# Kernel optimization log

Hardware: AMD Instinct MI355X
Metric: run time of the kernel (lower is better)

## Reference

```python
import jax, jax.numpy as jnp
import numpy as np

B, N, D, DH = 8, 2048, 1024, 64

def setup_inputs() -> dict:
    key = jax.random.key(0)
    ks = jax.random.split(key, 4)
    s = 1.0 / np.sqrt(D)
    return {
        "x": jax.random.normal(ks[0], (B, N, D), dtype=jnp.float32),
        "Wq": jax.random.normal(ks[1], (D, DH), dtype=jnp.float32) * s,
        "bq": jnp.zeros((DH,), dtype=jnp.float32),
        "Wk": jax.random.normal(ks[2], (D, DH), dtype=jnp.float32) * s,
        "bk": jnp.zeros((DH,), dtype=jnp.float32),
        "Wv": jax.random.normal(ks[3], (D, DH), dtype=jnp.float32) * s,
        "bv": jnp.zeros((DH,), dtype=jnp.float32),
    }

def reference(x, Wq, bq, Wk, bk, Wv, bv):
    # Projections: [B,N,DH]
    Q = x @ Wq + bq
    K = x @ Wk + bk
    V = x @ Wv + bv
    sqrt_dh = jnp.sqrt(jnp.asarray(DH, dtype=x.dtype))
    # scores[b,i,j] = Q_i . K_j  (original materializes [B,N,N,DH]; GEMM is equivalent math)
    att = jnp.einsum("bid,bjd->bij", Q, K) / sqrt_dh
    # NOTE: original softmaxes over dim=1 (the query/i axis), not the usual j axis.
    att = jax.nn.softmax(att, axis=1)
    # Dropout is identity in eval mode.
    return jnp.einsum("bij,bjd->bid", att, V)
```

## Files before the change

### kernel.cpp

```cpp
#include <hip/hip_runtime.h>
#include <math.h>

#define Bn  8
#define Nn  2048
#define Dn  1024
#define DHn 64

typedef __attribute__((ext_vector_type(8))) short bf16x8;
typedef __attribute__((ext_vector_type(4))) float f32x4;

static __device__ inline short f2bf(float f) {
    unsigned u = __builtin_bit_cast(unsigned, f);
    u += 0x7FFFu + ((u >> 16) & 1u);
    return (short)(u >> 16);
}
static __device__ inline bf16x8 pack8(float4 a, float4 b) {
    bf16x8 v;
    v[0] = f2bf(a.x); v[1] = f2bf(a.y); v[2] = f2bf(a.z); v[3] = f2bf(a.w);
    v[4] = f2bf(b.x); v[5] = f2bf(b.y); v[6] = f2bf(b.z); v[7] = f2bf(b.w);
    return v;
}

__global__ __launch_bounds__(256) void wt_kernel(
    const float* __restrict__ Wq, const float* __restrict__ Wk,
    const float* __restrict__ Wv, short* __restrict__ Wt)
{
    const int gn = blockIdx.x;
    const float* Wm = (gn < 64) ? Wq : (gn < 128 ? Wk : Wv);
    const int n = gn & 63;
    const int t = threadIdx.x;
#pragma unroll
    for (int r = 0; r < 4; ++r) {
        const int k = t * 4 + r;
        Wt[gn * Dn + k] = f2bf(Wm[k * DHn + n]);
    }
}

__global__ __launch_bounds__(256) void zero_kernel(float* __restrict__ out,
                                                   float* __restrict__ l)
{
    const int id = blockIdx.x * 256 + threadIdx.x;
    const float4 z = make_float4(0.f, 0.f, 0.f, 0.f);
    if (id < 262144) ((float4*)out)[id] = z;
    else             ((float4*)l)[id - 262144] = z;
}

__global__ __launch_bounds__(256) void qkv_kernel(
    const float* __restrict__ x, const short* __restrict__ Wt,
    const float* __restrict__ bq, const float* __restrict__ bk,
    const float* __restrict__ bv,
    short* __restrict__ Qb, short* __restrict__ Kb, short* __restrict__ Vt)
{
    __shared__ __attribute__((aligned(16))) short xs[64][72];

    const int t = threadIdx.x;
    const int w = t >> 6, lane = t & 63;
    const int c = lane & 15, quad = lane >> 4;
    const int rowbase = blockIdx.x * 64;
    const int r0 = t >> 3, kc = t & 7;

    float4 pf[4];
    {
        const float* p0 = &x[(size_t)(rowbase + r0) * Dn + kc * 8];
        pf[0] = *(const float4*)p0; pf[1] = *(const float4*)(p0 + 4);
        const float* p1 = &x[(size_t)(rowbase + r0 + 32) * Dn + kc * 8];
        pf[2] = *(const float4*)p1; pf[3] = *(const float4*)(p1 + 4);
    }

    f32x4 acc[4][3];
#pragma unroll
    for (int mt = 0; mt < 4; ++mt)
#pragma unroll
        for (int nt = 0; nt < 3; ++nt) acc[mt][nt] = (f32x4){0.f, 0.f, 0.f, 0.f};

    for (int kt = 0; kt < 16; ++kt) {
        __syncthreads();
        *(bf16x8*)&xs[r0][kc * 8]      = pack8(pf[0], pf[1]);
        *(bf16x8*)&xs[r0 + 32][kc * 8] = pack8(pf[2], pf[3]);
        __syncthreads();
        if (kt < 15) {
            const int k0n = (kt + 1) * 64;
            const float* p0 = &x[(size_t)(rowbase + r0) * Dn + k0n + kc * 8];
            pf[0] = *(const float4*)p0; pf[1] = *(const float4*)(p0 + 4);
            const float* p1 = &x[(size_t)(rowbase + r0 + 32) * Dn + k0n + kc * 8];
            pf[2] = *(const float4*)p1; pf[3] = *(const float4*)(p1 + 4);
        }
        const int k0 = kt * 64;
#pragma unroll
        for (int kk = 0; kk < 2; ++kk) {
            bf16x8 bfr[3];
#pragma unroll
            for (int nt = 0; nt < 3; ++nt)
                bfr[nt] = *(const bf16x8*)&Wt[(size_t)(w * 48 + nt * 16 + c) * Dn
                                              + k0 + kk * 32 + quad * 8];
#pragma unroll
            for (int mt = 0; mt < 4; ++mt) {
                const bf16x8 af = *(const bf16x8*)&xs[mt * 16 + c][kk * 32 + quad * 8];
#pragma unroll
                for (int nt = 0; nt < 3; ++nt)
                    acc[mt][nt] = __builtin_amdgcn_mfma_f32_16x16x32_bf16(
                        af, bfr[nt], acc[mt][nt], 0, 0, 0);
            }
        }
    }

#pragma unroll
    for (int nt = 0; nt < 3; ++nt) {
        const int col = w * 48 + nt * 16 + c;
        const int mat = col >> 6, cm = col & 63;
        const float bias = (mat == 0 ? bq : (mat == 1 ? bk : bv))[cm];
#pragma unroll
        for (int mt = 0; mt < 4; ++mt) {
#pragma unroll
            for (int r = 0; r < 4; ++r) {
                const int row = rowbase + mt * 16 + quad * 4 + r;
                const float o = acc[mt][nt][r] + bias;
                if (mat == 0)      Qb[(size_t)row * DHn + cm] = f2bf(o);
                else if (mat == 1) Kb[(size_t)row * DHn + cm] = f2bf(o * 0.125f);
                else {
                    const int b = row >> 11, i = row & (Nn - 1);
                    Vt[((size_t)b * DHn + cm) * Nn + i] = f2bf(o);
                }
            }
        }
    }
}

__global__ __launch_bounds__(256) void colsum_kernel(
    const short* __restrict__ Qb, const short* __restrict__ Kb,
    float* __restrict__ l)
{
    __shared__ __attribute__((aligned(16))) short Ks[64][72];
    __shared__ __attribute__((aligned(16))) short Qs[64][72];
    __shared__ float red[16][64];

    const int t = threadIdx.x;
    const int w = t >> 6, lane = t & 63;
    const int c = lane & 15, quad = lane >> 4;
    const int bid = blockIdx.x;
    const int b = bid >> 6, rem = bid & 63, jt = rem >> 1, half = rem & 1;
    const int jbase = jt * 64;
    const int r0 = t >> 3, kc = t & 7;

    *(bf16x8*)&Ks[r0][kc * 8]      = *(const bf16x8*)&Kb[((size_t)b * Nn + jbase + r0) * DHn + kc * 8];
    *(bf16x8*)&Ks[r0 + 32][kc * 8] = *(const bf16x8*)&Kb[((size_t)b * Nn + jbase + r0 + 32) * DHn + kc * 8];

    float lsum[4] = {0.f, 0.f, 0.f, 0.f};

    for (int it = 0; it < 16; ++it) {
        const int i0 = half * 1024 + it * 64;
        __syncthreads();
        *(bf16x8*)&Qs[r0][kc * 8]      = *(const bf16x8*)&Qb[((size_t)b * Nn + i0 + r0) * DHn + kc * 8];
        *(bf16x8*)&Qs[r0 + 32][kc * 8] = *(const bf16x8*)&Qb[((size_t)b * Nn + i0 + r0 + 32) * DHn + kc * 8];
        __syncthreads();

        bf16x8 af0 = *(const bf16x8*)&Qs[w * 16 + c][quad * 8];
        bf16x8 af1 = *(const bf16x8*)&Qs[w * 16 + c][32 + quad * 8];
#pragma unroll
        for (int nt = 0; nt < 4; ++nt) {
            f32x4 s = (f32x4){0.f, 0.f, 0.f, 0.f};
            s = __builtin_amdgcn_mfma_f32_16x16x32_bf16(
                af0, *(const bf16x8*)&Ks[nt * 16 + c][quad * 8], s, 0, 0, 0);
            s = __builtin_amdgcn_mfma_f32_16x16x32_bf16(
                af1, *(const bf16x8*)&Ks[nt * 16 + c][32 + quad * 8], s, 0, 0, 0);
            lsum[nt] += __expf(s[0]) + __expf(s[1]) + __expf(s[2]) + __expf(s[3]);
        }
    }

#pragma unroll
    for (int nt = 0; nt < 4; ++nt) red[w * 4 + quad][nt * 16 + c] = lsum[nt];
    __syncthreads();
    if (t < 64) {
        float s = 0.f;
#pragma unroll
        for (int r = 0; r < 16; ++r) s += red[r][t];
        atomicAdd(&l[(size_t)b * Nn + jbase + t], s);
    }
}

__global__ __launch_bounds__(256) void attnout_kernel(
    const short* __restrict__ Qb, const short* __restrict__ Kb,
    const short* __restrict__ Vt, const float* __restrict__ l,
    float* __restrict__ out)
{
    __shared__ __attribute__((aligned(16))) short Qs[64][72];
    __shared__ __attribute__((aligned(16))) short Ks[64][72];
    __shared__ __attribute__((aligned(16))) short Vst[64][72];
    __shared__ __attribute__((aligned(16))) short Ps[4][16][72];
    __shared__ float rls[64];

    const int t = threadIdx.x;
    const int w = t >> 6, lane = t & 63;
    const int c = lane & 15, quad = lane >> 4;
    const int bid = blockIdx.x;
    const int b = bid >> 6, rem = bid & 63, it = rem >> 1, half = rem & 1;
    const int ibase = it * 64;
    const int r0 = t >> 3, kc = t & 7;

    *(bf16x8*)&Qs[r0][kc * 8]      = *(const bf16x8*)&Qb[((size_t)b * Nn + ibase + r0) * DHn + kc * 8];
    *(bf16x8*)&Qs[r0 + 32][kc * 8] = *(const bf16x8*)&Qb[((size_t)b * Nn + ibase + r0 + 32) * DHn + kc * 8];

    f32x4 acc[4];
#pragma unroll
    for (int dn = 0; dn < 4; ++dn) acc[dn] = (f32x4){0.f, 0.f, 0.f, 0.f};

    for (int jt2 = 0; jt2 < 16; ++jt2) {
        const int jb = half * 1024 + jt2 * 64;
        __syncthreads();
        *(bf16x8*)&Ks[r0][kc * 8]       = *(const bf16x8*)&Kb[((size_t)b * Nn + jb + r0) * DHn + kc * 8];
        *(bf16x8*)&Ks[r0 + 32][kc * 8]  = *(const bf16x8*)&Kb[((size_t)b * Nn + jb + r0 + 32) * DHn + kc * 8];
        *(bf16x8*)&Vst[r0][kc * 8]      = *(const bf16x8*)&Vt[((size_t)b * DHn + r0) * Nn + jb + kc * 8];
        *(bf16x8*)&Vst[r0 + 32][kc * 8] = *(const bf16x8*)&Vt[((size_t)b * DHn + r0 + 32) * Nn + jb + kc * 8];
        if (t < 64) rls[t] = 1.0f / l[(size_t)b * Nn + jb + t];
        __syncthreads();

        bf16x8 aq0 = *(const bf16x8*)&Qs[w * 16 + c][quad * 8];
        bf16x8 aq1 = *(const bf16x8*)&Qs[w * 16 + c][32 + quad * 8];
#pragma unroll
        for (int nt = 0; nt < 4; ++nt) {
            f32x4 s = (f32x4){0.f, 0.f, 0.f, 0.f};
            s = __builtin_amdgcn_mfma_f32_16x16x32_bf16(
                aq0, *(const bf16x8*)&Ks[nt * 16 + c][quad * 8], s, 0, 0, 0);
            s = __builtin_amdgcn_mfma_f32_16x16x32_bf16(
                aq1, *(const bf16x8*)&Ks[nt * 16 + c][32 + quad * 8], s, 0, 0, 0);
            const float rl = rls[nt * 16 + c];
#pragma unroll
            for (int r = 0; r < 4; ++r)
                Ps[w][quad * 4 + r][nt * 16 + c] = f2bf(__expf(s[r]) * rl);
        }
        bf16x8 ap0 = *(const bf16x8*)&Ps[w][c][quad * 8];
        bf16x8 ap1 = *(const bf16x8*)&Ps[w][c][32 + quad * 8];
#pragma unroll
        for (int dn = 0; dn < 4; ++dn) {
            acc[dn] = __builtin_amdgcn_mfma_f32_16x16x32_bf16(
                ap0, *(const bf16x8*)&Vst[dn * 16 + c][quad * 8], acc[dn], 0, 0, 0);
            acc[dn] = __builtin_amdgcn_mfma_f32_16x16x32_bf16(
                ap1, *(const bf16x8*)&Vst[dn * 16 + c][32 + quad * 8], acc[dn], 0, 0, 0);
        }
    }

#pragma unroll
    for (int dn = 0; dn < 4; ++dn)
#pragma unroll
        for (int r = 0; r < 4; ++r)
            atomicAdd(&out[((size_t)b * Nn + ibase + w * 16 + quad * 4 + r) * DHn
                           + dn * 16 + c], acc[dn][r]);
}

extern "C" void kernel_launch(void* const* d_in, const int* in_sizes, int n_in,
                              void* d_out, int out_size, void* d_ws, size_t ws_size,
                              hipStream_t stream)
{
    const float* x  = (const float*)d_in[0];
    const float* Wq = (const float*)d_in[1];
    const float* bq = (const float*)d_in[2];
    const float* Wk = (const float*)d_in[3];
    const float* bk = (const float*)d_in[4];
    const float* Wv = (const float*)d_in[5];
    const float* bv = (const float*)d_in[6];
    float* out = (float*)d_out;

    char* ws = (char*)d_ws;
    short* Qb = (short*)(ws);
    short* Kb = (short*)(ws + (size_t)(1 << 21));
    short* Vt = (short*)(ws + (size_t)(2 << 21));
    short* Wt = (short*)(ws + (size_t)(3 << 21));
    float* lv = (float*)(ws + (size_t)(3 << 21) + (1 << 19));

    wt_kernel<<<dim3(192), dim3(256), 0, stream>>>(Wq, Wk, Wv, Wt);
    qkv_kernel<<<dim3(256), dim3(256), 0, stream>>>(x, Wt, bq, bk, bv, Qb, Kb, Vt);
    zero_kernel<<<dim3(1040), dim3(256), 0, stream>>>(out, lv);
    colsum_kernel<<<dim3(512), dim3(256), 0, stream>>>(Qb, Kb, lv);
    attnout_kernel<<<dim3(512), dim3(256), 0, stream>>>(Qb, Kb, Vt, lv, out);
}
```

Before: 174.3 us.

## Double grid sizes, drop LDS staging, fold softmax normalization into scaled V

The QKV projection now uses 32-row tiles, so it launches twice as many blocks. The column-sum and attention-output kernels split the reduction axis four ways instead of two, doubling their grids. Both kernels now read Q, K and V fragments straight from global memory into registers instead of staging them through shared memory with barriers. The per-column 1/l normalization moves out of the attention inner loop into a separate vscale kernel that rescales V in place, at the cost of one extra launch and an extra bf16 rounding of V. More split-axis blocks also means more atomic adds into the output.

New measurement: 219.1 us. 25.7% more time.

```diff
diff --git a/kernel.cpp b/kernel.cpp
--- a/kernel.cpp
+++ b/kernel.cpp
@@ -13,6 +13,10 @@
     unsigned u = __builtin_bit_cast(unsigned, f);
     u += 0x7FFFu + ((u >> 16) & 1u);
     return (short)(u >> 16);
+}
+static __device__ inline float bf2f(short s) {
+    unsigned u = ((unsigned)(unsigned short)s) << 16;
+    return __builtin_bit_cast(float, u);
 }
 static __device__ inline bf16x8 pack8(float4 a, float4 b) {
     bf16x8 v;
@@ -51,39 +55,33 @@
     const float* __restrict__ bv,
     short* __restrict__ Qb, short* __restrict__ Kb, short* __restrict__ Vt)
 {
-    __shared__ __attribute__((aligned(16))) short xs[64][72];
+    __shared__ __attribute__((aligned(16))) short xs[32][72];
 
     const int t = threadIdx.x;
     const int w = t >> 6, lane = t & 63;
     const int c = lane & 15, quad = lane >> 4;
-    const int rowbase = blockIdx.x * 64;
+    const int rowbase = blockIdx.x * 32;
     const int r0 = t >> 3, kc = t & 7;
 
-    float4 pf[4];
+    float4 pf[2];
     {
         const float* p0 = &x[(size_t)(rowbase + r0) * Dn + kc * 8];
         pf[0] = *(const float4*)p0; pf[1] = *(const float4*)(p0 + 4);
-        const float* p1 = &x[(size_t)(rowbase + r0 + 32) * Dn + kc * 8];
-        pf[2] = *(const float4*)p1; pf[3] = *(const float4*)(p1 + 4);
-    }
-
-    f32x4 acc[4][3];
-#pragma unroll
-    for (int mt = 0; mt < 4; ++mt)
+    }
+
+    f32x4 acc[2][3];
+#pragma unroll
+    for (int mt = 0; mt < 2; ++mt)
 #pragma unroll
         for (int nt = 0; nt < 3; ++nt) acc[mt][nt] = (f32x4){0.f, 0.f, 0.f, 0.f};
 
     for (int kt = 0; kt < 16; ++kt) {
         __syncthreads();
-        *(bf16x8*)&xs[r0][kc * 8]      = pack8(pf[0], pf[1]);
-        *(bf16x8*)&xs[r0 + 32][kc * 8] = pack8(pf[2], pf[3]);
+        *(bf16x8*)&xs[r0][kc * 8] = pack8(pf[0], pf[1]);
         __syncthreads();
         if (kt < 15) {
-            const int k0n = (kt + 1) * 64;
-            const float* p0 = &x[(size_t)(rowbase + r0) * Dn + k0n + kc * 8];
+            const float* p0 = &x[(size_t)(rowbase + r0) * Dn + (kt + 1) * 64 + kc * 8];
             pf[0] = *(const float4*)p0; pf[1] = *(const float4*)(p0 + 4);
-            const float* p1 = &x[(size_t)(rowbase + r0 + 32) * Dn + k0n + kc * 8];
-            pf[2] = *(const float4*)p1; pf[3] = *(const float4*)(p1 + 4);
         }
         const int k0 = kt * 64;
 #pragma unroll
@@ -94,7 +92,7 @@
                 bfr[nt] = *(const bf16x8*)&Wt[(size_t)(w * 48 + nt * 16 + c) * Dn
                                               + k0 + kk * 32 + quad * 8];
 #pragma unroll
-            for (int mt = 0; mt < 4; ++mt) {
+            for (int mt = 0; mt < 2; ++mt) {
                 const bf16x8 af = *(const bf16x8*)&xs[mt * 16 + c][kk * 32 + quad * 8];
 #pragma unroll
                 for (int nt = 0; nt < 3; ++nt)
@@ -110,7 +108,7 @@
         const int mat = col >> 6, cm = col & 63;
         const float bias = (mat == 0 ? bq : (mat == 1 ? bk : bv))[cm];
 #pragma unroll
-        for (int mt = 0; mt < 4; ++mt) {
+        for (int mt = 0; mt < 2; ++mt) {
 #pragma unroll
             for (int r = 0; r < 4; ++r) {
                 const int row = rowbase + mt * 16 + quad * 4 + r;
@@ -130,40 +128,36 @@
     const short* __restrict__ Qb, const short* __restrict__ Kb,
     float* __restrict__ l)
 {
-    __shared__ __attribute__((aligned(16))) short Ks[64][72];
-    __shared__ __attribute__((aligned(16))) short Qs[64][72];
     __shared__ float red[16][64];
 
     const int t = threadIdx.x;
     const int w = t >> 6, lane = t & 63;
     const int c = lane & 15, quad = lane >> 4;
     const int bid = blockIdx.x;
-    const int b = bid >> 6, rem = bid & 63, jt = rem >> 1, half = rem & 1;
+    const int b = bid >> 7, rem = bid & 127, jt = rem >> 2, s = rem & 3;
     const int jbase = jt * 64;
-    const int r0 = t >> 3, kc = t & 7;
-
-    *(bf16x8*)&Ks[r0][kc * 8]      = *(const bf16x8*)&Kb[((size_t)b * Nn + jbase + r0) * DHn + kc * 8];
-    *(bf16x8*)&Ks[r0 + 32][kc * 8] = *(const bf16x8*)&Kb[((size_t)b * Nn + jbase + r0 + 32) * DHn + kc * 8];
+
+    bf16x8 kb[4][2];
+#pragma unroll
+    for (int nt = 0; nt < 4; ++nt)
+#pragma unroll
+        for (int kk = 0; kk < 2; ++kk)
+            kb[nt][kk] = *(const bf16x8*)&Kb[((size_t)b * Nn + jbase + nt * 16 + c) * DHn
+                                             + kk * 32 + quad * 8];
 
     float lsum[4] = {0.f, 0.f, 0.f, 0.f};
 
-    for (int it = 0; it < 16; ++it) {
-        const int i0 = half * 1024 + it * 64;
-        __syncthreads();
-        *(bf16x8*)&Qs[r0][kc * 8]      = *(const bf16x8*)&Qb[((size_t)b * Nn + i0 + r0) * DHn + kc * 8];
-        *(bf16x8*)&Qs[r0 + 32][kc * 8] = *(const bf16x8*)&Qb[((size_t)b * Nn + i0 + r0 + 32) * DHn + kc * 8];
-        __syncthreads();
-
-        bf16x8 af0 = *(const bf16x8*)&Qs[w * 16 + c][quad * 8];
-        bf16x8 af1 = *(const bf16x8*)&Qs[w * 16 + c][32 + quad * 8];
+#pragma unroll
+    for (int ch = 0; ch < 8; ++ch) {
+        const int i0 = s * 512 + (ch * 4 + w) * 16;
+        const bf16x8 aq0 = *(const bf16x8*)&Qb[((size_t)b * Nn + i0 + c) * DHn + quad * 8];
+        const bf16x8 aq1 = *(const bf16x8*)&Qb[((size_t)b * Nn + i0 + c) * DHn + 32 + quad * 8];
 #pragma unroll
         for (int nt = 0; nt < 4; ++nt) {
-            f32x4 s = (f32x4){0.f, 0.f, 0.f, 0.f};
-            s = __builtin_amdgcn_mfma_f32_16x16x32_bf16(
-                af0, *(const bf16x8*)&Ks[nt * 16 + c][quad * 8], s, 0, 0, 0);
-            s = __builtin_amdgcn_mfma_f32_16x16x32_bf16(
-                af1, *(const bf16x8*)&Ks[nt * 16 + c][32 + quad * 8], s, 0, 0, 0);
-            lsum[nt] += __expf(s[0]) + __expf(s[1]) + __expf(s[2]) + __expf(s[3]);
+            f32x4 sv = (f32x4){0.f, 0.f, 0.f, 0.f};
+            sv = __builtin_amdgcn_mfma_f32_16x16x32_bf16(aq0, kb[nt][0], sv, 0, 0, 0);
+            sv = __builtin_amdgcn_mfma_f32_16x16x32_bf16(aq1, kb[nt][1], sv, 0, 0, 0);
+            lsum[nt] += __expf(sv[0]) + __expf(sv[1]) + __expf(sv[2]) + __expf(sv[3]);
         }
     }
 
@@ -171,71 +165,73 @@
     for (int nt = 0; nt < 4; ++nt) red[w * 4 + quad][nt * 16 + c] = lsum[nt];
     __syncthreads();
     if (t < 64) {
-        float s = 0.f;
-#pragma unroll
-        for (int r = 0; r < 16; ++r) s += red[r][t];
-        atomicAdd(&l[(size_t)b * Nn + jbase + t], s);
-    }
+        float sum = 0.f;
+#pragma unroll
+        for (int r = 0; r < 16; ++r) sum += red[r][t];
+        atomicAdd(&l[(size_t)b * Nn + jbase + t], sum);
+    }
+}
+
+__global__ __launch_bounds__(256) void vscale_kernel(
+    short* __restrict__ Vt, const float* __restrict__ l)
+{
+    const int row = blockIdx.x;
+    const int b = row >> 6;
+    const int t = threadIdx.x;
+    const int j0 = t * 8;
+    bf16x8 v = *(const bf16x8*)&Vt[(size_t)row * Nn + j0];
+    const float4 l0 = *(const float4*)&l[(size_t)b * Nn + j0];
+    const float4 l1 = *(const float4*)&l[(size_t)b * Nn + j0 + 4];
+    const float rl[8] = {1.f / l0.x, 1.f / l0.y, 1.f / l0.z, 1.f / l0.w,
+                         1.f / l1.x, 1.f / l1.y, 1.f / l1.z, 1.f / l1.w};
+    bf16x8 o;
+#pragma unroll
+    for (int e = 0; e < 8; ++e) o[e] = f2bf(bf2f(v[e]) * rl[e]);
+    *(bf16x8*)&Vt[(size_t)row * Nn + j0] = o;
 }
 
 __global__ __launch_bounds__(256) void attnout_kernel(
     const short* __restrict__ Qb, const short* __restrict__ Kb,
-    const short* __restrict__ Vt, const float* __restrict__ l,
-    float* __restrict__ out)
-{
-    __shared__ __attribute__((aligned(16))) short Qs[64][72];
-    __shared__ __attribute__((aligned(16))) short Ks[64][72];
-    __shared__ __attribute__((aligned(16))) short Vst[64][72];
+    const short* __restrict__ Vt, float* __restrict__ out)
+{
     __shared__ __attribute__((aligned(16))) short Ps[4][16][72];
-    __shared__ float rls[64];
 
     const int t = threadIdx.x;
     const int w = t >> 6, lane = t & 63;
     const int c = lane & 15, quad = lane >> 4;
     const int bid = blockIdx.x;
-    const int b = bid >> 6, rem = bid & 63, it = rem >> 1, half = rem & 1;
+    const int b = bid >> 7, rem = bid & 127, it = rem >> 2, s = rem & 3;
     const int ibase = it * 64;
-    const int r0 = t >> 3, kc = t & 7;
-
-    *(bf16x8*)&Qs[r0][kc * 8]      = *(const bf16x8*)&Qb[((size_t)b * Nn + ibase + r0) * DHn + kc * 8];
-    *(bf16x8*)&Qs[r0 + 32][kc * 8] = *(const bf16x8*)&Qb[((size_t)b * Nn + ibase + r0 + 32) * DHn + kc * 8];
+
+    const bf16x8 aq0 = *(const bf16x8*)&Qb[((size_t)b * Nn + ibase + w * 16 + c) * DHn + quad * 8];
+    const bf16x8 aq1 = *(const bf16x8*)&Qb[((size_t)b * Nn + ibase + w * 16 + c) * DHn + 32 + quad * 8];
 
     f32x4 acc[4];
 #pragma unroll
     for (int dn = 0; dn < 4; ++dn) acc[dn] = (f32x4){0.f, 0.f, 0.f, 0.f};
 
-    for (int jt2 = 0; jt2 < 16; ++jt2) {
-        const int jb = half * 1024 + jt2 * 64;
-        __syncthreads();
-        *(bf16x8*)&Ks[r0][kc * 8]       = *(const bf16x8*)&Kb[((size_t)b * Nn + jb + r0) * DHn + kc * 8];
-        *(bf16x8*)&Ks[r0 + 32][kc * 8]  = *(const bf16x8*)&Kb[((size_t)b * Nn + jb + r0 + 32) * DHn + kc * 8];
-        *(bf16x8*)&Vst[r0][kc * 8]      = *(const bf16x8*)&Vt[((size_t)b * DHn + r0) * Nn + jb + kc * 8];
-        *(bf16x8*)&Vst[r0 + 32][kc * 8] = *(const bf16x8*)&Vt[((size_t)b * DHn + r0 + 32) * Nn + jb + kc * 8];
-        if (t < 64) rls[t] = 1.0f / l[(size_t)b * Nn + jb + t];
-        __syncthreads();
-
-        bf16x8 aq0 = *(const bf16x8*)&Qs[w * 16 + c][quad * 8];
-        bf16x8 aq1 = *(const bf16x8*)&Qs[w * 16 + c][32 + quad * 8];
+#pragma unroll 2
+    for (int ch = 0; ch < 8; ++ch) {
+        const int jb = s * 512 + ch * 64;
 #pragma unroll
         for (int nt = 0; nt < 4; ++nt) {
-            f32x4 s = (f32x4){0.f, 0.f, 0.f, 0.f};
-            s = __builtin_amdgcn_mfma_f32_16x16x32_bf16(
-                aq0, *(const bf16x8*)&Ks[nt * 16 + c][quad * 8], s, 0, 0, 0);
-            s = __builtin_amdgcn_mfma_f32_16x16x32_bf16(
-                aq1, *(const bf16x8*)&Ks[nt * 16 + c][32 + quad * 8], s, 0, 0, 0);
-            const float rl = rls[nt * 16 + c];
+            const bf16x8 kb0 = *(const bf16x8*)&Kb[((size_t)b * Nn + jb + nt * 16 + c) * DHn + quad * 8];
+            const bf16x8 kb1 = *(const bf16x8*)&Kb[((size_t)b * Nn + jb + nt * 16 + c) * DHn + 32 + quad * 8];
+            f32x4 sv = (f32x4){0.f, 0.f, 0.f, 0.f};
+            sv = __builtin_amdgcn_mfma_f32_16x16x32_bf16(aq0, kb0, sv, 0, 0, 0);
+            sv = __builtin_amdgcn_mfma_f32_16x16x32_bf16(aq1, kb1, sv, 0, 0, 0);
 #pragma unroll
             for (int r = 0; r < 4; ++r)
-                Ps[w][quad * 4 + r][nt * 16 + c] = f2bf(__expf(s[r]) * rl);
-        }
-        bf16x8 ap0 = *(const bf16x8*)&Ps[w][c][quad * 8];
-        bf16x8 ap1 = *(const bf16x8*)&Ps[w][c][32 + quad * 8];
+                Ps[w][quad * 4 + r][nt * 16 + c] = f2bf(__expf(sv[r]));
+        }
+        const bf16x8 ap0 = *(const bf16x8*)&Ps[w][c][quad * 8];
+        const bf16x8 ap1 = *(const bf16x8*)&Ps[w][c][32 + quad * 8];
 #pragma unroll
         for (int dn = 0; dn < 4; ++dn) {
-            acc[dn] = __builtin_amdgcn_mfma_f32_16x16x32_bf16(
-                ap0, *(const bf16x8*)&Vst[dn * 16 + c][quad * 8], acc[dn], 0, 0, 0);
-            acc[dn] = __builtin_amdgcn_mfma_f32_16x16x32_bf16(
-                ap1, *(const bf16x8*)&Vst[dn * 16 + c][32 + quad * 8], acc[dn], 0, 0, 0);
+            const bf16x8 vb0 = *(const bf16x8*)&Vt[((size_t)b * DHn + dn * 16 + c) * Nn + jb + quad * 8];
+            const bf16x8 vb1 = *(const bf16x8*)&Vt[((size_t)b * DHn + dn * 16 + c) * Nn + jb + 32 + quad * 8];
+            acc[dn] = __builtin_amdgcn_mfma_f32_16x16x32_bf16(ap0, vb0, acc[dn], 0, 0, 0);
+            acc[dn] = __builtin_amdgcn_mfma_f32_16x16x32_bf16(ap1, vb1, acc[dn], 0, 0, 0);
         }
     }
 
@@ -267,9 +263,10 @@
     short* Wt = (short*)(ws + (size_t)(3 << 21));
     float* lv = (float*)(ws + (size_t)(3 << 21) + (1 << 19));
 
+    zero_kernel<<<dim3(1040), dim3(256), 0, stream>>>(out, lv);
     wt_kernel<<<dim3(192), dim3(256), 0, stream>>>(Wq, Wk, Wv, Wt);
-    qkv_kernel<<<dim3(256), dim3(256), 0, stream>>>(x, Wt, bq, bk, bv, Qb, Kb, Vt);
-    zero_kernel<<<dim3(1040), dim3(256), 0, stream>>>(out, lv);
-    colsum_kernel<<<dim3(512), dim3(256), 0, stream>>>(Qb, Kb, lv);
-    attnout_kernel<<<dim3(512), dim3(256), 0, stream>>>(Qb, Kb, Vt, lv, out);
-}
+    qkv_kernel<<<dim3(512), dim3(256), 0, stream>>>(x, Wt, bq, bk, bv, Qb, Kb, Vt);
+    colsum_kernel<<<dim3(1024), dim3(256), 0, stream>>>(Qb, Kb, lv);
+    vscale_kernel<<<dim3(512), dim3(256), 0, stream>>>(Vt, lv);
+    attnout_kernel<<<dim3(1024), dim3(256), 0, stream>>>(Qb, Kb, Vt, out);
+}
```
